# Kernel optimization log

Measured on AMD Instinct MI355X. Metric: run time of the kernel, lower is better.

## Reference

```python
import jax, jax.numpy as jnp
import numpy as np
from jax import lax

B, L, D = 2, 2048, 128
H, HD = 8, 32
WIN = 3

def setup_inputs() -> dict:
    key = jax.random.key(0)
    ks = jax.random.split(key, 7)
    s = 0.05
    return {
        "x":  jax.random.normal(ks[0], (B, L, D), jnp.float32),
        "pe": jax.random.normal(ks[1], (L, D), jnp.float32) * s,
        "Wq": jax.random.normal(ks[2], (D, H * HD), jnp.float32) * s,
        "bq": jnp.zeros((H * HD,), jnp.float32),
        "Wk": jax.random.normal(ks[3], (D, H * HD), jnp.float32) * s,
        "bk": jnp.zeros((H * HD,), jnp.float32),
        "Wv": jax.random.normal(ks[4], (D, H), jnp.float32) * s,
    }

def reference(x, pe, Wq, bq, Wk, bk, Wv):
    b, l, d = x.shape
    h = Wv.shape[1]
    hd = Wq.shape[1] // h
    xp = x + pe                                   # (B,L,D)
    # split heads: Dense output columns [i*hd:(i+1)*hd] -> head i
    q = (xp @ Wq + bq).reshape(b, l, h, hd).transpose(2, 0, 1, 3)  # (H,B,L,hd)
    k = (xp @ Wk + bk).reshape(b, l, h, hd).transpose(2, 0, 1, 3)  # (H,B,L,hd)
    v = jax.nn.sigmoid(x @ Wv).transpose(2, 0, 1)                  # (H,B,L)

    attn = jnp.einsum('hbqd,hbkd->hbqk', q, k) * (float(hd) ** -0.5)
    attn = jax.nn.softmax(attn, axis=-1)          # (H,B,L,L)

    # band_part(0,-1) + diag_part(k=(0,L-1)) (RIGHT_LEFT align) + transpose + reverse(-2,-1)
    # collapses to the skew-gather: R[p, m] = attn[L-1-p-m, L-1-p] for p+m <= L-1 else 0
    p = jnp.arange(l)[:, None]                    # (L,1)
    m = jnp.arange(l)[None, :]                    # (1,L)
    ii = l - 1 - p - m                            # row index  (L,L)
    jj = jnp.broadcast_to(l - 1 - p, (l, l))      # col index  (L,L)
    valid = (ii >= 0)
    R = attn[:, :, jnp.where(valid, ii, 0), jj] * valid.astype(attn.dtype)  # (H,B,L,L)

    R = R * v[:, :, :, None]                      # gate by value, broadcast over distance axis

    # TF avg_pool excludes padding from the divisor
    sums = lax.reduce_window(R, 0.0, lax.add, (1, 1, 1, WIN), (1, 1, 1, 1), 'SAME')
    cnt = lax.reduce_window(jnp.ones((l,), R.dtype), 0.0, lax.add, (WIN,), (1,), 'SAME')
    pooled = sums / cnt                           # (H,B,L,L)

    # global mode: sum over position axis, -> (B, L_dist, H)
    out = pooled.sum(axis=2).transpose(1, 2, 0)
    return out
```

## Files before the change

### kernel.cpp

```cpp
#include <hip/hip_runtime.h>
#include <hip/hip_bf16.h>

#define LSEQ 2048
#define BB 2
#define DD 128
#define HH 8
#define HD 32

#define FPSCALE 524288.0f
#define RFPSCALE (1.0f / 524288.0f)
#define DENSCALE 65536.0f
#define QSCALE 0.25503486f

typedef __bf16 bf8_t __attribute__((ext_vector_type(8)));
typedef __bf16 bf4_t __attribute__((ext_vector_type(4)));
typedef float f4_t __attribute__((ext_vector_type(4)));

__global__ __launch_bounds__(256) void k_A(const float* __restrict__ x,
                                           const float* __restrict__ pe,
                                           const float* __restrict__ Wq,
                                           const float* __restrict__ Wk,
                                           const float* __restrict__ Wv,
                                           const float* __restrict__ bq,
                                           const float* __restrict__ bk,
                                           float* __restrict__ w,
                                           __bf16* __restrict__ Qb,
                                           __bf16* __restrict__ Kb,
                                           int* __restrict__ Si,
                                           int* __restrict__ denI) {
    __shared__ __align__(16) char smem[34816];
    int gb = blockIdx.x;
    int tid = threadIdx.x;

    if (gb < 512) {
        __bf16* xs = (__bf16*)smem;
        __bf16* Wt = (__bf16*)(smem + 64 * 136 * 2);
        int jr = gb >> 3, y = gb & 7;
        int row0 = jr * 64;
        bool isK = y >= 4;
        int cbase = (y & 3) * 64;
        const float* W = isK ? Wk : Wq;

        #pragma unroll
        for (int i = 0; i < 8; i++) {
            int idx4 = tid + i * 256;
            int row = idx4 >> 5, col4 = idx4 & 31;
            float4 xv = ((const float4*)x)[row0 * 32 + idx4];
            float4 pv = ((const float4*)pe)[((row0 + row) & (LSEQ - 1)) * 32 + col4];
            bf4_t o = {(__bf16)(xv.x + pv.x), (__bf16)(xv.y + pv.y),
                       (__bf16)(xv.z + pv.z), (__bf16)(xv.w + pv.w)};
            *(bf4_t*)&xs[row * 136 + col4 * 4] = o;
        }
        #pragma unroll
        for (int i = 0; i < 8; i++) {
            int idx4 = tid + i * 256;
            int d = idx4 >> 4, c4 = (idx4 & 15) * 4;
            float4 wv4 = *(const float4*)(W + d * 256 + cbase + c4);
            Wt[(c4 + 0) * 136 + d] = (__bf16)wv4.x;
            Wt[(c4 + 1) * 136 + d] = (__bf16)wv4.y;
            Wt[(c4 + 2) * 136 + d] = (__bf16)wv4.z;
            Wt[(c4 + 3) * 136 + d] = (__bf16)wv4.w;
        }
        __syncthreads();

        int wid = tid >> 6, lane = tid & 63;
        int lm = lane & 15, lq = lane >> 4;
        int c0loc = wid * 16;
        f4_t acc0 = {0,0,0,0}, acc1 = {0,0,0,0}, acc2 = {0,0,0,0}, acc3 = {0,0,0,0};
        #pragma unroll
        for (int s = 0; s < 4; s++) {
            bf8_t bw = *(const bf8_t*)&Wt[(c0loc + lm) * 136 + lq * 8 + s * 32];
            bf8_t a0 = *(const bf8_t*)&xs[(0  + lm) * 136 + lq * 8 + s * 32];
            bf8_t a1 = *(const bf8_t*)&xs[(16 + lm) * 136 + lq * 8 + s * 32];
            bf8_t a2 = *(const bf8_t*)&xs[(32 + lm) * 136 + lq * 8 + s * 32];
            bf8_t a3 = *(const bf8_t*)&xs[(48 + lm) * 136 + lq * 8 + s * 32];
            acc0 = __builtin_amdgcn_mfma_f32_16x16x32_bf16(a0, bw, acc0, 0, 0, 0);
            acc1 = __builtin_amdgcn_mfma_f32_16x16x32_bf16(a1, bw, acc1, 0, 0, 0);
            acc2 = __builtin_amdgcn_mfma_f32_16x16x32_bf16(a2, bw, acc2, 0, 0, 0);
            acc3 = __builtin_amdgcn_mfma_f32_16x16x32_bf16(a3, bw, acc3, 0, 0, 0);
        }
        int c = cbase + c0loc + lm;
        float bv = (isK ? bk : bq)[c];
        float qs = isK ? 1.f : QSCALE;
        __bf16* Out = isK ? Kb : Qb;
        int h = c >> 5, hd = c & 31;
        f4_t accs[4] = {acc0, acc1, acc2, acc3};
        #pragma unroll
        for (int rs = 0; rs < 4; rs++) {
            #pragma unroll
            for (int r = 0; r < 4; r++) {
                int row = row0 + rs * 16 + lq * 4 + r;
                int b_ = row >> 11, l = row & (LSEQ - 1);
                Out[((h * BB + b_) * LSEQ + l) * HD + hd] =
                    (__bf16)((accs[rs][r] + bv) * qs);
            }
        }
    } else if (gb < 640) {
        float* xsf = (float*)smem;
        float* wvf = (float*)(smem + 32 * 132 * 4);
        int r0 = (gb - 512) * 32;
        for (int i = 0; i < 16; i++) {
            int idx = tid + i * 256;
            xsf[(idx >> 7) * 132 + (idx & 127)] = x[r0 * 128 + idx];
        }
        for (int i = 0; i < 4; i++) {
            int idx = tid + i * 256;
            wvf[idx] = Wv[idx];
        }
        __syncthreads();
        int rl = tid >> 3, h = tid & 7;
        float acc = 0.f;
        #pragma unroll 8
        for (int d = 0; d < 128; d++) acc += xsf[rl * 132 + d] * wvf[d * 8 + h];
        float sg = 1.f / (1.f + __expf(-acc));
        int r = r0 + rl;
        int b = r >> 11, l = r & (LSEQ - 1);
        w[(h * BB + b) * LSEQ + (LSEQ - 1 - l)] = sg;
    } else if (gb < 672) {
        int4 z = {0, 0, 0, 0};
        ((int4*)Si)[(gb - 640) * 256 + tid] = z;
    } else {
        int4 z = {0, 0, 0, 0};
        ((int4*)denI)[(gb - 672) * 256 + tid] = z;
    }
}

__global__ __launch_bounds__(256) void k_den(const __bf16* __restrict__ Qb,
                                             const __bf16* __restrict__ Kb,
                                             int* __restrict__ denI) {
    int hb = blockIdx.z;
    int q0 = blockIdx.y * 64;
    int kbase = blockIdx.x * 512;
    int wid = threadIdx.x >> 6, lane = threadIdx.x & 63;
    int lm = lane & 15, lq = lane >> 4;
    int qw0 = q0 + wid * 16;

    bf8_t aq = *(const bf8_t*)(Qb + (hb * LSEQ + qw0 + lm) * HD + lq * 8);
    const __bf16* Khb = Kb + hb * LSEQ * HD;

    float dsum[4] = {0.f, 0.f, 0.f, 0.f};
    #pragma unroll 4
    for (int s = 0; s < 32; s++) {
        bf8_t bk_ = *(const bf8_t*)(Khb + (kbase + s * 16 + lm) * HD + lq * 8);
        f4_t z = {0.f, 0.f, 0.f, 0.f};
        f4_t sc = __builtin_amdgcn_mfma_f32_16x16x32_bf16(aq, bk_, z, 0, 0, 0);
        #pragma unroll
        for (int r = 0; r < 4; r++) dsum[r] += exp2f(sc[r]);
    }
    #pragma unroll
    for (int r = 0; r < 4; r++) {
        float v = dsum[r];
        v += __shfl_xor(v, 1);
        v += __shfl_xor(v, 2);
        v += __shfl_xor(v, 4);
        v += __shfl_xor(v, 8);
        dsum[r] = v;
    }
    if (lm == 0) {
        #pragma unroll
        for (int r = 0; r < 4; r++)
            atomicAdd(&denI[hb * LSEQ + qw0 + lq * 4 + r],
                      __float2int_rn(dsum[r] * DENSCALE));
    }
}

__global__ __launch_bounds__(256) void k_scat(const __bf16* __restrict__ Qb,
                                              const __bf16* __restrict__ Kb,
                                              const float* __restrict__ w,
                                              const int* __restrict__ denI,
                                              int* __restrict__ S) {
    int hb = blockIdx.z;
    int q0 = blockIdx.y * 64;
    int kc0 = blockIdx.x * 256;
    if (kc0 + 256 <= q0) return;

    __shared__ int Sloc[4 * 320];
    __shared__ float wt[256];
    int tid = threadIdx.x;
    for (int i = tid; i < 1280; i += 256) Sloc[i] = 0;
    wt[tid] = w[hb * LSEQ + kc0 + tid] * FPSCALE;

    int wid = tid >> 6, lane = tid & 63;
    int lm = lane & 15, lq = lane >> 4;
    int qw0 = q0 + wid * 16;
    bf8_t aq = *(const bf8_t*)(Qb + (hb * LSEQ + qw0 + lm) * HD + lq * 8);
    float rdv[4];
    #pragma unroll
    for (int r = 0; r < 4; r++)
        rdv[r] = DENSCALE / (float)denI[hb * LSEQ + qw0 + lq * 4 + r];
    __syncthreads();

    const __bf16* Khb = Kb + hb * LSEQ * HD;
    int mbase = kc0 - q0 - 63;
    int qrow = qw0 + lq * 4;
    int* mySloc = Sloc + wid * 320;

    int sub_start = (qw0 > kc0) ? ((qw0 - kc0) >> 4) : 0;

    {
        int k0s = kc0 + sub_start * 16;
        bf8_t bk_ = *(const bf8_t*)(Khb + (k0s + lm) * HD + lq * 8);
        f4_t z = {0.f, 0.f, 0.f, 0.f};
        f4_t sc = __builtin_amdgcn_mfma_f32_16x16x32_bf16(aq, bk_, z, 0, 0, 0);
        float wvs = wt[sub_start * 16 + lm];
        int kcol = k0s + lm;
        #pragma unroll
        for (int r = 0; r < 4; r++) {
            int m = kcol - (qrow + r);
            if (m >= 0) {
                int iv = __float2int_rn(exp2f(sc[r]) * rdv[r] * wvs);
                atomicAdd(&mySloc[m - mbase], iv);
            }
        }
    }
    #pragma unroll 4
    for (int sub = sub_start + 1; sub < 16; sub++) {
        int k0s = kc0 + sub * 16;
        bf8_t bk_ = *(const bf8_t*)(Khb + (k0s + lm) * HD + lq * 8);
        f4_t z = {0.f, 0.f, 0.f, 0.f};
        f4_t sc = __builtin_amdgcn_mfma_f32_16x16x32_bf16(aq, bk_, z, 0, 0, 0);
        float wvs = wt[sub * 16 + lm];
        int kcol = k0s + lm;
        #pragma unroll
        for (int r = 0; r < 4; r++) {
            int m = kcol - (qrow + r);
            int iv = __float2int_rn(exp2f(sc[r]) * rdv[r] * wvs);
            atomicAdd(&mySloc[m - mbase], iv);
        }
    }
    __syncthreads();
    for (int i = tid; i < 320; i += 256) {
        int m = mbase + i;
        int v = Sloc[i] + Sloc[320 + i] + Sloc[640 + i] + Sloc[960 + i];
        if (m >= 0 && m < LSEQ && v != 0)
            atomicAdd(&S[hb * LSEQ + m], v);
    }
}

__global__ __launch_bounds__(256) void k_out(const int* __restrict__ S,
                                             float* __restrict__ out) {
    int idx = blockIdx.x * 256 + threadIdx.x;
    int h = idx & 7;
    int m = (idx >> 3) & (LSEQ - 1);
    int b = idx >> 14;
    const int* Sr = S + (h * BB + b) * LSEQ;
    float s = (float)Sr[m];
    float cnt = 3.f;
    if (m > 0) s += (float)Sr[m - 1]; else cnt = 2.f;
    if (m < LSEQ - 1) s += (float)Sr[m + 1]; else cnt = 2.f;
    out[idx] = s * RFPSCALE / cnt;
}

extern "C" void kernel_launch(void* const* d_in, const int* in_sizes, int n_in,
                              void* d_out, int out_size, void* d_ws, size_t ws_size,
                              hipStream_t stream) {
    const float* x  = (const float*)d_in[0];
    const float* pe = (const float*)d_in[1];
    const float* Wq = (const float*)d_in[2];
    const float* bq = (const float*)d_in[3];
    const float* Wk = (const float*)d_in[4];
    const float* bk = (const float*)d_in[5];
    const float* Wv = (const float*)d_in[6];
    float* out = (float*)d_out;

    char* ws = (char*)d_ws;
    int*    Si   = (int*)(ws);
    float*  w    = (float*)(ws + 131072);
    __bf16* Qb   = (__bf16*)(ws + 262144);
    __bf16* Kb   = (__bf16*)(ws + 262144 + 2097152);
    int*    denI = (int*)(ws + 262144 + 4194304);

    k_A<<<704, 256, 0, stream>>>(x, pe, Wq, Wk, Wv, bq, bk, w, Qb, Kb, Si, denI);
    k_den<<<dim3(4, 32, 16), 256, 0, stream>>>(Qb, Kb, denI);
    k_scat<<<dim3(8, 32, 16), 256, 0, stream>>>(Qb, Kb, w, denI, Si);
    k_out<<<128, 256, 0, stream>>>(Si, out);
}
```

Measured before the change: 128.1 us.

## Reuse K tiles across two Q tiles, privatize LDS bins per quad, fold scaling into exp2

k_den now computes two 16-row Q tiles per wave against each loaded K fragment, halving the grid and the K reloads. k_scat splits the shared histogram into 16 private copies (one per wave and lane-quad, padded stride) to cut LDS atomic contention. It also folds the reciprocal denominator and gate weight into the exp2 argument as log2 terms, replacing two multiplies with adds. The log2 of the gate weight needs w > 0, which holds for a sigmoid output, and the extra LDS copies raise shared memory use and the final reduction cost.

```diff
diff --git a/kernel.cpp b/kernel.cpp
--- a/kernel.cpp
+++ b/kernel.cpp
@@ -129,41 +129,49 @@
                                              const __bf16* __restrict__ Kb,
                                              int* __restrict__ denI) {
     int hb = blockIdx.z;
-    int q0 = blockIdx.y * 64;
+    int q0 = blockIdx.y * 128;
     int kbase = blockIdx.x * 512;
     int wid = threadIdx.x >> 6, lane = threadIdx.x & 63;
     int lm = lane & 15, lq = lane >> 4;
-    int qw0 = q0 + wid * 16;
-
-    bf8_t aq = *(const bf8_t*)(Qb + (hb * LSEQ + qw0 + lm) * HD + lq * 8);
+    int qa = q0 + wid * 16;
+    int qb2 = qa + 64;
+
+    bf8_t aqa = *(const bf8_t*)(Qb + (hb * LSEQ + qa + lm) * HD + lq * 8);
+    bf8_t aqb = *(const bf8_t*)(Qb + (hb * LSEQ + qb2 + lm) * HD + lq * 8);
     const __bf16* Khb = Kb + hb * LSEQ * HD;
 
-    float dsum[4] = {0.f, 0.f, 0.f, 0.f};
+    float dsa[4] = {0.f, 0.f, 0.f, 0.f};
+    float dsb[4] = {0.f, 0.f, 0.f, 0.f};
     #pragma unroll 4
     for (int s = 0; s < 32; s++) {
         bf8_t bk_ = *(const bf8_t*)(Khb + (kbase + s * 16 + lm) * HD + lq * 8);
         f4_t z = {0.f, 0.f, 0.f, 0.f};
-        f4_t sc = __builtin_amdgcn_mfma_f32_16x16x32_bf16(aq, bk_, z, 0, 0, 0);
-        #pragma unroll
-        for (int r = 0; r < 4; r++) dsum[r] += exp2f(sc[r]);
+        f4_t sa = __builtin_amdgcn_mfma_f32_16x16x32_bf16(aqa, bk_, z, 0, 0, 0);
+        f4_t sb = __builtin_amdgcn_mfma_f32_16x16x32_bf16(aqb, bk_, z, 0, 0, 0);
+        #pragma unroll
+        for (int r = 0; r < 4; r++) { dsa[r] += exp2f(sa[r]); dsb[r] += exp2f(sb[r]); }
     }
     #pragma unroll
     for (int r = 0; r < 4; r++) {
-        float v = dsum[r];
-        v += __shfl_xor(v, 1);
-        v += __shfl_xor(v, 2);
-        v += __shfl_xor(v, 4);
-        v += __shfl_xor(v, 8);
-        dsum[r] = v;
+        float va = dsa[r], vb = dsb[r];
+        va += __shfl_xor(va, 1); vb += __shfl_xor(vb, 1);
+        va += __shfl_xor(va, 2); vb += __shfl_xor(vb, 2);
+        va += __shfl_xor(va, 4); vb += __shfl_xor(vb, 4);
+        va += __shfl_xor(va, 8); vb += __shfl_xor(vb, 8);
+        dsa[r] = va; dsb[r] = vb;
     }
     if (lm == 0) {
         #pragma unroll
-        for (int r = 0; r < 4; r++)
-            atomicAdd(&denI[hb * LSEQ + qw0 + lq * 4 + r],
-                      __float2int_rn(dsum[r] * DENSCALE));
-    }
-}
-
+        for (int r = 0; r < 4; r++) {
+            atomicAdd(&denI[hb * LSEQ + qa + lq * 4 + r],
+                      __float2int_rn(dsa[r] * DENSCALE));
+            atomicAdd(&denI[hb * LSEQ + qb2 + lq * 4 + r],
+                      __float2int_rn(dsb[r] * DENSCALE));
+        }
+    }
+}
+
+#define SSTRIDE 332
 __global__ __launch_bounds__(256) void k_scat(const __bf16* __restrict__ Qb,
                                               const __bf16* __restrict__ Kb,
                                               const float* __restrict__ w,
@@ -174,26 +182,26 @@
     int kc0 = blockIdx.x * 256;
     if (kc0 + 256 <= q0) return;
 
-    __shared__ int Sloc[4 * 320];
-    __shared__ float wt[256];
+    __shared__ int Sloc[16 * SSTRIDE];
+    __shared__ float lwt[256];
     int tid = threadIdx.x;
-    for (int i = tid; i < 1280; i += 256) Sloc[i] = 0;
-    wt[tid] = w[hb * LSEQ + kc0 + tid] * FPSCALE;
+    for (int i = tid; i < 16 * SSTRIDE; i += 256) Sloc[i] = 0;
+    lwt[tid] = log2f(w[hb * LSEQ + kc0 + tid]);
 
     int wid = tid >> 6, lane = tid & 63;
     int lm = lane & 15, lq = lane >> 4;
     int qw0 = q0 + wid * 16;
     bf8_t aq = *(const bf8_t*)(Qb + (hb * LSEQ + qw0 + lm) * HD + lq * 8);
-    float rdv[4];
+    float lrd[4];
     #pragma unroll
     for (int r = 0; r < 4; r++)
-        rdv[r] = DENSCALE / (float)denI[hb * LSEQ + qw0 + lq * 4 + r];
+        lrd[r] = log2f(DENSCALE * FPSCALE / (float)denI[hb * LSEQ + qw0 + lq * 4 + r]);
     __syncthreads();
 
     const __bf16* Khb = Kb + hb * LSEQ * HD;
     int mbase = kc0 - q0 - 63;
     int qrow = qw0 + lq * 4;
-    int* mySloc = Sloc + wid * 320;
+    int* mySloc = Sloc + (wid * 4 + lq) * SSTRIDE;
 
     int sub_start = (qw0 > kc0) ? ((qw0 - kc0) >> 4) : 0;
 
@@ -202,13 +210,13 @@
         bf8_t bk_ = *(const bf8_t*)(Khb + (k0s + lm) * HD + lq * 8);
         f4_t z = {0.f, 0.f, 0.f, 0.f};
         f4_t sc = __builtin_amdgcn_mfma_f32_16x16x32_bf16(aq, bk_, z, 0, 0, 0);
-        float wvs = wt[sub_start * 16 + lm];
+        float lw = lwt[sub_start * 16 + lm];
         int kcol = k0s + lm;
         #pragma unroll
         for (int r = 0; r < 4; r++) {
             int m = kcol - (qrow + r);
             if (m >= 0) {
-                int iv = __float2int_rn(exp2f(sc[r]) * rdv[r] * wvs);
+                int iv = __float2int_rn(exp2f(sc[r] + lrd[r] + lw));
                 atomicAdd(&mySloc[m - mbase], iv);
             }
         }
@@ -219,19 +227,21 @@
         bf8_t bk_ = *(const bf8_t*)(Khb + (k0s + lm) * HD + lq * 8);
         f4_t z = {0.f, 0.f, 0.f, 0.f};
         f4_t sc = __builtin_amdgcn_mfma_f32_16x16x32_bf16(aq, bk_, z, 0, 0, 0);
-        float wvs = wt[sub * 16 + lm];
+        float lw = lwt[sub * 16 + lm];
         int kcol = k0s + lm;
         #pragma unroll
         for (int r = 0; r < 4; r++) {
             int m = kcol - (qrow + r);
-            int iv = __float2int_rn(exp2f(sc[r]) * rdv[r] * wvs);
+            int iv = __float2int_rn(exp2f(sc[r] + lrd[r] + lw));
             atomicAdd(&mySloc[m - mbase], iv);
         }
     }
     __syncthreads();
     for (int i = tid; i < 320; i += 256) {
         int m = mbase + i;
-        int v = Sloc[i] + Sloc[320 + i] + Sloc[640 + i] + Sloc[960 + i];
+        int v = 0;
+        #pragma unroll
+        for (int s = 0; s < 16; s++) v += Sloc[s * SSTRIDE + i];
         if (m >= 0 && m < LSEQ && v != 0)
             atomicAdd(&S[hb * LSEQ + m], v);
     }
@@ -271,7 +281,7 @@
     int*    denI = (int*)(ws + 262144 + 4194304);
 
     k_A<<<704, 256, 0, stream>>>(x, pe, Wq, Wk, Wv, bq, bk, w, Qb, Kb, Si, denI);
-    k_den<<<dim3(4, 32, 16), 256, 0, stream>>>(Qb, Kb, denI);
+    k_den<<<dim3(4, 16, 16), 256, 0, stream>>>(Qb, Kb, denI);
     k_scat<<<dim3(8, 32, 16), 256, 0, stream>>>(Qb, Kb, w, denI, Si);
     k_out<<<128, 256, 0, stream>>>(Si, out);
 }
```

Result: slower. 131.4 us (+2.6%).
